# Kernel optimization log

Measured on AMD Instinct MI355X. Metric: run time of the kernel, lower is better.

## Reference

```python
import jax, jax.numpy as jnp
import numpy as np

T, B, E, H = 512, 64, 256, 256


def setup_inputs() -> dict:
    key = jax.random.key(0)
    ks = jax.random.split(key, 14)
    def p(k, shape, s=0.05):
        return jax.random.normal(k, shape, dtype=jnp.float32) * s
    return {
        "inputs": jax.random.normal(ks[0], (T, B, E), dtype=jnp.float32),
        # attention params (nn.Parameter torch.randn -> unit scale)
        "rot": jax.random.normal(ks[1], (E, E), dtype=jnp.float32),
        "ent": jax.random.normal(ks[2], (E, E), dtype=jnp.float32),
        # gate linears: stored as (in, out) so y = x @ W + b (same math as torch Linear)
        "Wf": p(ks[3], (E + H, H)), "bf": jnp.zeros((H,), jnp.float32),
        "Wi": p(ks[4], (E + H, H)), "bi": jnp.zeros((H,), jnp.float32),
        "Wu": p(ks[5], (E + H, H)), "bu": jnp.zeros((H,), jnp.float32),
        "Wo": p(ks[6], (E + H, H)), "bo": jnp.zeros((H,), jnp.float32),
        "Wc": p(ks[7], (E, H)),     "bc": jnp.zeros((H,), jnp.float32),
    }


def reference(inputs, rot, ent, Wf, bf, Wi, bi, Wu, bu, Wo, bo, Wc, bc):
    t, b, e = inputs.shape
    h = Wf.shape[1]
    # --- one-shot self-attention (ClassicalSelfAttention) ---
    inp = inputs.transpose(1, 0, 2)                       # [B,T,E]
    q = jnp.einsum('bte,ef->btf', inp, rot)
    k = jnp.einsum('bte,ef->btf', inp, ent)
    scores = jax.nn.softmax(jnp.einsum('btf,bsf->bts', q, k) / jnp.sqrt(jnp.float32(e)), axis=-1)
    context = jnp.einsum('bts,bse->bte', scores, inp).transpose(1, 0, 2)  # [T,B,E]
    # context projection is time-invariant -> precompute as one big GEMM
    ctx_proj = context @ Wc + bc                          # [T,B,H]
    # --- recurrent LSTM cell over time via scan ---
    def step(carry, xs):
        hx, cx = carry
        x, cp = xs
        combined = jnp.concatenate([x, hx + cp], axis=1)  # [B,E+H]
        f = jax.nn.sigmoid(combined @ Wf + bf)
        i = jax.nn.sigmoid(combined @ Wi + bi)
        g = jnp.tanh(combined @ Wu + bu)
        o = jax.nn.sigmoid(combined @ Wo + bo)
        cx = f * cx + i * g
        hx = o * jnp.tanh(cx)
        return (hx, cx), hx
    hx0 = jnp.zeros((b, h), inputs.dtype)
    cx0 = jnp.zeros((b, h), inputs.dtype)
    (hx, cx), outputs = jax.lax.scan(step, (hx0, cx0), (inputs, ctx_proj))
    return outputs, hx, cx
```

## Files before the change

kernel.cpp:

```cpp
#include <hip/hip_runtime.h>

#define T_ 512
#define B_ 64
#define E_ 256
#define H_ 256

typedef __attribute__((ext_vector_type(8))) short short8_t;
typedef __attribute__((ext_vector_type(4))) float floatx4;

__device__ __forceinline__ unsigned short f2bf(float f) {
  unsigned int u = __float_as_uint(f);
  u += 0x7FFFu + ((u >> 16) & 1u);
  return (unsigned short)(u >> 16);
}
__device__ __forceinline__ float bf2f(unsigned short s) {
  return __uint_as_float(((unsigned int)s) << 16);
}
__device__ __forceinline__ float fast_tanh(float x) {
  float e = __expf(-2.0f * x);
  return 2.0f / (1.0f + e) - 1.0f;
}

__global__ __launch_bounds__(256) void qk_kernel(
    const float* __restrict__ inp, const float* __restrict__ rot,
    const float* __restrict__ ent, float* __restrict__ qo, float* __restrict__ ko)
{
  __shared__ __align__(16) float As[16][136];
  __shared__ __align__(16) float B1[16][68];
  __shared__ __align__(16) float B2[16][68];
  const int tid = threadIdx.x;
  const int m0 = blockIdx.y * 128, n0 = blockIdx.x * 64;
  const int lk = tid & 15, lm = tid >> 4;
  const int ln = tid & 63, lkb = tid >> 6;
  const int tx = tid & 15, ty = tid >> 4;
  float acc1[8][4], acc2[8][4];
#pragma unroll
  for (int i = 0; i < 8; ++i)
#pragma unroll
    for (int j = 0; j < 4; ++j) { acc1[i][j] = 0.f; acc2[i][j] = 0.f; }

  for (int k0 = 0; k0 < 256; k0 += 16) {
    __syncthreads();
#pragma unroll
    for (int p = 0; p < 8; ++p) {
      int m = lm + p * 16;
      As[lk][m] = inp[(size_t)(m0 + m) * 256 + k0 + lk];
    }
#pragma unroll
    for (int p = 0; p < 4; ++p) {
      int kk = lkb + p * 4;
      B1[kk][ln] = rot[(size_t)(k0 + kk) * 256 + n0 + ln];
      B2[kk][ln] = ent[(size_t)(k0 + kk) * 256 + n0 + ln];
    }
    __syncthreads();
#pragma unroll
    for (int kk = 0; kk < 16; ++kk) {
      floatx4 a_lo = *(const floatx4*)&As[kk][ty * 8];
      floatx4 a_hi = *(const floatx4*)&As[kk][ty * 8 + 4];
      floatx4 b1v = *(const floatx4*)&B1[kk][tx * 4];
      floatx4 b2v = *(const floatx4*)&B2[kk][tx * 4];
#pragma unroll
      for (int i = 0; i < 4; ++i) {
        float alo = a_lo[i], ahi = a_hi[i];
#pragma unroll
        for (int j = 0; j < 4; ++j) {
          acc1[i][j]     += alo * b1v[j];
          acc1[i + 4][j] += ahi * b1v[j];
          acc2[i][j]     += alo * b2v[j];
          acc2[i + 4][j] += ahi * b2v[j];
        }
      }
    }
  }
#pragma unroll
  for (int i = 0; i < 8; ++i) {
    size_t row = (size_t)(m0 + ty * 8 + i);
    float4 v1 = make_float4(acc1[i][0], acc1[i][1], acc1[i][2], acc1[i][3]);
    float4 v2 = make_float4(acc2[i][0], acc2[i][1], acc2[i][2], acc2[i][3]);
    *(float4*)&qo[row * 256 + n0 + tx * 4] = v1;
    *(float4*)&ko[row * 256 + n0 + tx * 4] = v2;
  }
}

__global__ __launch_bounds__(256) void scores_kernel(
    const float* __restrict__ q, const float* __restrict__ k, float* __restrict__ S)
{
  __shared__ __align__(16) float As[16][136];
  __shared__ __align__(16) float Bs[16][68];
  const int tid = threadIdx.x;
  const int b = blockIdx.z;
  const int m0 = blockIdx.y * 128, n0 = blockIdx.x * 64;
  const int lk = tid & 15, lm = tid >> 4;
  const int tx = tid & 15, ty = tid >> 4;
  float acc[8][4];
#pragma unroll
  for (int i = 0; i < 8; ++i)
#pragma unroll
    for (int j = 0; j < 4; ++j) acc[i][j] = 0.f;

  const float* Ab = q + (size_t)b * 256;
  const float* Bb = k + (size_t)b * 256;
  for (int k0 = 0; k0 < 256; k0 += 16) {
    __syncthreads();
#pragma unroll
    for (int p = 0; p < 8; ++p) {
      int m = lm + p * 16;
      As[lk][m] = Ab[(size_t)(m0 + m) * 16384 + k0 + lk];
    }
#pragma unroll
    for (int p = 0; p < 4; ++p) {
      int n = lm + p * 16;
      Bs[lk][n] = Bb[(size_t)(n0 + n) * 16384 + k0 + lk];
    }
    __syncthreads();
#pragma unroll
    for (int kk = 0; kk < 16; ++kk) {
      floatx4 a_lo = *(const floatx4*)&As[kk][ty * 8];
      floatx4 a_hi = *(const floatx4*)&As[kk][ty * 8 + 4];
      floatx4 bv = *(const floatx4*)&Bs[kk][tx * 4];
#pragma unroll
      for (int i = 0; i < 4; ++i) {
        float alo = a_lo[i], ahi = a_hi[i];
#pragma unroll
        for (int j = 0; j < 4; ++j) {
          acc[i][j]     += alo * bv[j];
          acc[i + 4][j] += ahi * bv[j];
        }
      }
    }
  }
#pragma unroll
  for (int i = 0; i < 8; ++i) {
    size_t off = (size_t)b * 262144 + (size_t)(m0 + ty * 8 + i) * 512 + n0 + tx * 4;
    float4 v = make_float4(acc[i][0] * 0.0625f, acc[i][1] * 0.0625f,
                           acc[i][2] * 0.0625f, acc[i][3] * 0.0625f);
    *(float4*)&S[off] = v;
  }
}

__global__ __launch_bounds__(256) void softmax_kernel(float* __restrict__ S)
{
  float* p = S + (size_t)blockIdx.x * 512;
  const int tid = threadIdx.x;
  float x0 = p[tid], x1 = p[tid + 256];
  float m = fmaxf(x0, x1);
#pragma unroll
  for (int off = 32; off > 0; off >>= 1) m = fmaxf(m, __shfl_xor(m, off));
  __shared__ float red[8];
  const int wv = tid >> 6;
  if ((tid & 63) == 0) red[wv] = m;
  __syncthreads();
  m = fmaxf(fmaxf(red[0], red[1]), fmaxf(red[2], red[3]));
  float e0 = __expf(x0 - m);
  float e1 = __expf(x1 - m);
  float s = e0 + e1;
#pragma unroll
  for (int off = 32; off > 0; off >>= 1) s += __shfl_xor(s, off);
  if ((tid & 63) == 0) red[4 + wv] = s;
  __syncthreads();
  s = red[4] + red[5] + red[6] + red[7];
  float r = 1.0f / s;
  p[tid] = e0 * r;
  p[tid + 256] = e1 * r;
}

__global__ __launch_bounds__(256) void context_kernel(
    const float* __restrict__ P, const float* __restrict__ inp, float* __restrict__ ctx)
{
  __shared__ __align__(16) float As[16][136];
  __shared__ __align__(16) float Bs[16][68];
  const int tid = threadIdx.x;
  const int b = blockIdx.z;
  const int m0 = blockIdx.y * 128, e0 = blockIdx.x * 64;
  const int lk = tid & 15, lm = tid >> 4;
  const int ln = tid & 63, lkb = tid >> 6;
  const int tx = tid & 15, ty = tid >> 4;
  float acc[8][4];
#pragma unroll
  for (int i = 0; i < 8; ++i)
#pragma unroll
    for (int j = 0; j < 4; ++j) acc[i][j] = 0.f;

  const float* Ab = P + (size_t)b * 262144;
  for (int k0 = 0; k0 < 512; k0 += 16) {
    __syncthreads();
#pragma unroll
    for (int p = 0; p < 8; ++p) {
      int m = lm + p * 16;
      As[lk][m] = Ab[(size_t)(m0 + m) * 512 + k0 + lk];
    }
#pragma unroll
    for (int p = 0; p < 4; ++p) {
      int kk = lkb + p * 4;
      Bs[kk][ln] = inp[(size_t)(k0 + kk) * 16384 + b * 256 + e0 + ln];
    }
    __syncthreads();
#pragma unroll
    for (int kk = 0; kk < 16; ++kk) {
      floatx4 a_lo = *(const floatx4*)&As[kk][ty * 8];
      floatx4 a_hi = *(const floatx4*)&As[kk][ty * 8 + 4];
      floatx4 bv = *(const floatx4*)&Bs[kk][tx * 4];
#pragma unroll
      for (int i = 0; i < 4; ++i) {
        float alo = a_lo[i], ahi = a_hi[i];
#pragma unroll
        for (int j = 0; j < 4; ++j) {
          acc[i][j]     += alo * bv[j];
          acc[i + 4][j] += ahi * bv[j];
        }
      }
    }
  }
#pragma unroll
  for (int i = 0; i < 8; ++i) {
    size_t off = (size_t)(m0 + ty * 8 + i) * 16384 + (size_t)b * 256 + e0 + tx * 4;
    float4 v = make_float4(acc[i][0], acc[i][1], acc[i][2], acc[i][3]);
    *(float4*)&ctx[off] = v;
  }
}

__global__ __launch_bounds__(256) void cp_kernel(
    const float* __restrict__ ctx, const float* __restrict__ Wc,
    const float* __restrict__ bc, float* __restrict__ cp)
{
  __shared__ __align__(16) float As[16][136];
  __shared__ __align__(16) float Bs[16][68];
  const int tid = threadIdx.x;
  const int m0 = blockIdx.y * 128, n0 = blockIdx.x * 64;
  const int lk = tid & 15, lm = tid >> 4;
  const int ln = tid & 63, lkb = tid >> 6;
  const int tx = tid & 15, ty = tid >> 4;
  float acc[8][4];
#pragma unroll
  for (int i = 0; i < 8; ++i)
#pragma unroll
    for (int j = 0; j < 4; ++j) acc[i][j] = 0.f;

  for (int k0 = 0; k0 < 256; k0 += 16) {
    __syncthreads();
#pragma unroll
    for (int p = 0; p < 8; ++p) {
      int m = lm + p * 16;
      As[lk][m] = ctx[(size_t)(m0 + m) * 256 + k0 + lk];
    }
#pragma unroll
    for (int p = 0; p < 4; ++p) {
      int kk = lkb + p * 4;
      Bs[kk][ln] = Wc[(size_t)(k0 + kk) * 256 + n0 + ln];
    }
    __syncthreads();
#pragma unroll
    for (int kk = 0; kk < 16; ++kk) {
      floatx4 a_lo = *(const floatx4*)&As[kk][ty * 8];
      floatx4 a_hi = *(const floatx4*)&As[kk][ty * 8 + 4];
      floatx4 bv = *(const floatx4*)&Bs[kk][tx * 4];
#pragma unroll
      for (int i = 0; i < 4; ++i) {
        float alo = a_lo[i], ahi = a_hi[i];
#pragma unroll
        for (int j = 0; j < 4; ++j) {
          acc[i][j]     += alo * bv[j];
          acc[i + 4][j] += ahi * bv[j];
        }
      }
    }
  }
  float b0 = bc[n0 + tx * 4 + 0], b1 = bc[n0 + tx * 4 + 1];
  float b2 = bc[n0 + tx * 4 + 2], b3 = bc[n0 + tx * 4 + 3];
#pragma unroll
  for (int i = 0; i < 8; ++i) {
    size_t row = (size_t)(m0 + ty * 8 + i);
    float4 v = make_float4(acc[i][0] + b0, acc[i][1] + b1, acc[i][2] + b2, acc[i][3] + b3);
    *(float4*)&cp[row * 256 + n0 + tx * 4] = v;
  }
}

__global__ __launch_bounds__(256) void pack_w(
    const float* __restrict__ Wf, const float* __restrict__ Wi,
    const float* __restrict__ Wu, const float* __restrict__ Wo,
    const float* __restrict__ bfv, const float* __restrict__ biv,
    const float* __restrict__ buv, const float* __restrict__ bov,
    unsigned short* __restrict__ Wt, float* __restrict__ bcat)
{
  const int n = blockIdx.x;
  const int g = n >> 8, h = n & 255;
  const float* W = (g == 0) ? Wf : (g == 1) ? Wi : (g == 2) ? Wu : Wo;
  const float* bb = (g == 0) ? bfv : (g == 1) ? biv : (g == 2) ? buv : bov;
  for (int k = threadIdx.x; k < 512; k += 256)
    Wt[(size_t)n * 512 + k] = f2bf(W[(size_t)k * 256 + h]);
  if (threadIdx.x == 0) bcat[n] = bb[h];
}

__global__ __launch_bounds__(256) void gemm_pre(
    const float* __restrict__ x, const float* __restrict__ cp,
    const unsigned short* __restrict__ Wt, const float* __restrict__ bcat,
    unsigned short* __restrict__ pre)
{
  __shared__ __align__(16) unsigned short As[64 * 40];
  __shared__ __align__(16) unsigned short Bs[64 * 40];
  const int tid = threadIdx.x;
  const int n0 = blockIdx.x * 64, m0 = blockIdx.y * 64;
  const int lane = tid & 63, wv = tid >> 6;
  const int lm = lane & 15, qd = lane >> 4;
  const int sr = tid >> 2, sk = (tid & 3) * 8;
  floatx4 acc[4] = {{0.f,0.f,0.f,0.f},{0.f,0.f,0.f,0.f},
                    {0.f,0.f,0.f,0.f},{0.f,0.f,0.f,0.f}};
  for (int k0 = 0; k0 < 512; k0 += 32) {
    const float* Asrc = (k0 < 256)
        ? (x  + (size_t)(m0 + sr) * 256 + k0 + sk)
        : (cp + (size_t)(m0 + sr) * 256 + (k0 - 256) + sk);
    float4 a0 = *(const float4*)Asrc;
    float4 a1 = *(const float4*)(Asrc + 4);
    short8_t av;
    av[0] = (short)f2bf(a0.x); av[1] = (short)f2bf(a0.y);
    av[2] = (short)f2bf(a0.z); av[3] = (short)f2bf(a0.w);
    av[4] = (short)f2bf(a1.x); av[5] = (short)f2bf(a1.y);
    av[6] = (short)f2bf(a1.z); av[7] = (short)f2bf(a1.w);
    short8_t bv = *(const short8_t*)&Wt[(size_t)(n0 + sr) * 512 + k0 + sk];
    *(short8_t*)&As[sr * 40 + sk] = av;
    *(short8_t*)&Bs[sr * 40 + sk] = bv;
    __syncthreads();
    short8_t af = *(const short8_t*)&As[(wv * 16 + lm) * 40 + qd * 8];
#pragma unroll
    for (int nt = 0; nt < 4; ++nt) {
      short8_t bf = *(const short8_t*)&Bs[(nt * 16 + lm) * 40 + qd * 8];
      acc[nt] = __builtin_amdgcn_mfma_f32_16x16x32_bf16(af, bf, acc[nt], 0, 0, 0);
    }
    __syncthreads();
  }
#pragma unroll
  for (int nt = 0; nt < 4; ++nt) {
    int col = n0 + nt * 16 + lm;
    float bb = bcat[col];
    int col2 = ((col & 255) << 2) | (col >> 8);
#pragma unroll
    for (int r = 0; r < 4; ++r) {
      int row = m0 + wv * 16 + qd * 4 + r;
      pre[(size_t)row * 1024 + col2] = f2bf(acc[nt][r] + bb);
    }
  }
}

__global__ __launch_bounds__(512, 2) void scan_kernel(
    const unsigned short* __restrict__ pre,
    const unsigned short* __restrict__ Wt,
    float* __restrict__ out)
{
  __shared__ __align__(16) unsigned short ldsB[8 * 18 * 512];
  __shared__ __align__(16) unsigned short hl[2][9 * 264];
  const int tid = threadIdx.x;
  const int bg = blockIdx.x;
  const int lane = tid & 63;
  const int w = tid >> 6;
  const int qd = lane >> 4;
  const int lm = lane & 15;

  {
    unsigned long long* z = (unsigned long long*)hl;
    for (int i = tid; i < 1188; i += 512) z[i] = 0ull;
  }

  short8_t wreg[46];
#pragma unroll
  for (int nt = 0; nt < 8; ++nt) {
#pragma unroll
    for (int kc = 0; kc < 8; ++kc) {
      const int idx = nt * 8 + kc;
      const int g = nt >> 1, cg2 = nt & 1;
      short8_t v = *(const short8_t*)&Wt[
          (size_t)(g * 256 + w * 32 + cg2 * 16 + lm) * 512 + 256 + kc * 32 + qd * 8];
      if (idx < 46) wreg[idx] = v;
      else *(short8_t*)&ldsB[(w * 18 + (idx - 46)) * 512 + lane * 8] = v;
    }
  }

  const int rh = lane >> 5;
  const int cg2d = (lane >> 4) & 1;
  const int c15 = lane & 15;
  const int hc = w * 32 + cg2d * 16 + c15;
  const int srcl = rh * 16 + c15;
  const int arow = (lm < 8) ? lm : 8;
  const int aoff = arow * 264 + qd * 8;

  const unsigned long long* pq = (const unsigned long long*)pre;
  float cst[4] = {0.f, 0.f, 0.f, 0.f};

  __syncthreads();

#pragma unroll 1
  for (int t = 0; t < 512; ++t) {
    const unsigned short* hbR = hl[t & 1];

    unsigned long long pcur[4];
    {
      size_t base = (size_t)(t * 64 + bg * 8 + rh * 4) * 256 + hc;
#pragma unroll
      for (int r = 0; r < 4; ++r)
        pcur[r] = pq[base + (size_t)r * 256];
    }

    floatx4 acc[8];
#pragma unroll
    for (int nt = 0; nt < 8; ++nt) acc[nt] = {0.f, 0.f, 0.f, 0.f};
#pragma unroll
    for (int kc = 0; kc < 8; ++kc) {
      short8_t av = *(const short8_t*)&hbR[aoff + kc * 32];
#pragma unroll
      for (int nt = 0; nt < 8; ++nt) {
        const int idx = nt * 8 + kc;
        short8_t bf;
        if (idx < 46) bf = wreg[idx];
        else bf = *(const short8_t*)&ldsB[(w * 18 + (idx - 46)) * 512 + lane * 8];
        acc[nt] = __builtin_amdgcn_mfma_f32_16x16x32_bf16(av, bf, acc[nt], 0, 0, 0);
      }
    }

    unsigned short* hbW = hl[(t + 1) & 1];
#pragma unroll
    for (int r = 0; r < 4; ++r) {
      float vg[4];
#pragma unroll
      for (int g = 0; g < 4; ++g) {
        float v0 = __shfl(acc[g * 2 + 0][r], srcl);
        float v1 = __shfl(acc[g * 2 + 1][r], srcl);
        vg[g] = cg2d ? v1 : v0;
      }
      unsigned long long pv = pcur[r];
      float xf = vg[0] + bf2f((unsigned short)pv);
      float xi = vg[1] + bf2f((unsigned short)(pv >> 16));
      float xu = vg[2] + bf2f((unsigned short)(pv >> 32));
      float xo = vg[3] + bf2f((unsigned short)(pv >> 48));
      float fg = 1.0f / (1.0f + __expf(-xf));
      float ig = 1.0f / (1.0f + __expf(-xi));
      float gg = fast_tanh(xu);
      float og = 1.0f / (1.0f + __expf(-xo));
      float cc = fg * cst[r] + ig * gg;
      cst[r] = cc;
      float hh = og * fast_tanh(cc);
      const int lr = rh * 4 + r;
      hbW[lr * 264 + hc] = f2bf(hh);
      out[(size_t)t * 16384 + (size_t)(bg * 8 + lr) * 256 + hc] = hh;
      if (t == 511) {
        const size_t hoff = (size_t)512 * 16384 + (size_t)(bg * 8 + lr) * 256 + hc;
        out[hoff] = hh;
        out[hoff + 16384] = cc;
      }
    }
    __syncthreads();
  }
}

extern "C" void kernel_launch(void* const* d_in, const int* in_sizes, int n_in,
                              void* d_out, int out_size, void* d_ws, size_t ws_size,
                              hipStream_t stream)
{
  const float* inputs = (const float*)d_in[0];
  const float* rot = (const float*)d_in[1];
  const float* ent = (const float*)d_in[2];
  const float* Wf = (const float*)d_in[3];
  const float* bf_ = (const float*)d_in[4];
  const float* Wi = (const float*)d_in[5];
  const float* bi_ = (const float*)d_in[6];
  const float* Wu = (const float*)d_in[7];
  const float* bu_ = (const float*)d_in[8];
  const float* Wo = (const float*)d_in[9];
  const float* bo_ = (const float*)d_in[10];
  const float* Wc = (const float*)d_in[11];
  const float* bc_ = (const float*)d_in[12];
  float* out = (float*)d_out;

  char* ws = (char*)d_ws;
  float* q  = (float*)(ws);
  float* kb = (float*)(ws + (size_t)32 * 1024 * 1024);
  float* S  = (float*)(ws + (size_t)64 * 1024 * 1024);
  unsigned short* pre = (unsigned short*)S;
  float* ctx = q;
  float* cp  = kb;
  unsigned short* Wcat = (unsigned short*)ws;
  float* bcat = (float*)(ws + (size_t)1048576);

  qk_kernel<<<dim3(4, 256), 256, 0, stream>>>(inputs, rot, ent, q, kb);
  scores_kernel<<<dim3(8, 4, 64), 256, 0, stream>>>(q, kb, S);
  softmax_kernel<<<dim3(32768), 256, 0, stream>>>(S);
  context_kernel<<<dim3(4, 4, 64), 256, 0, stream>>>(S, inputs, ctx);
  cp_kernel<<<dim3(4, 256), 256, 0, stream>>>(ctx, Wc, bc_, cp);
  pack_w<<<dim3(1024), 256, 0, stream>>>(Wf, Wi, Wu, Wo, bf_, bi_, bu_, bo_,
                                         Wcat, bcat);
  gemm_pre<<<dim3(16, 512), 256, 0, stream>>>(inputs, cp, Wcat, bcat, pre);
  scan_kernel<<<dim3(8), 512, 0, stream>>>(pre, Wcat, out);
}
```

Measured before the change: 2.064 ms.

## Restructure LSTM scan to 4 blocks of 16 waves streaming weights from global

The recurrent scan now runs 4 blocks of 1024 threads, each handling 16 batch rows with 16 waves, and each wave computes all four gates for 16 hidden columns. The gate values therefore land in the same lane and the cross-lane shuffles go away. Weights are no longer kept in registers and LDS. Instead they are reloaded from global/L2 every timestep, double-buffered one k-chunk ahead. This removes the shuffle and gate-assembly overhead and the LDS weight staging, at the cost of repeated weight loads from cache on the serial critical path and fewer parallel blocks.

```diff
diff --git a/kernel.cpp b/kernel.cpp
--- a/kernel.cpp
+++ b/kernel.cpp
@@ -341,13 +341,12 @@
   }
 }
 
-__global__ __launch_bounds__(512, 2) void scan_kernel(
+__global__ __launch_bounds__(1024, 4) void scan_kernel(
     const unsigned short* __restrict__ pre,
     const unsigned short* __restrict__ Wt,
     float* __restrict__ out)
 {
-  __shared__ __align__(16) unsigned short ldsB[8 * 18 * 512];
-  __shared__ __align__(16) unsigned short hl[2][9 * 264];
+  __shared__ __align__(16) unsigned short hl[2][16 * 264];
   const int tid = threadIdx.x;
   const int bg = blockIdx.x;
   const int lane = tid & 63;
@@ -357,79 +356,75 @@
 
   {
     unsigned long long* z = (unsigned long long*)hl;
-    for (int i = tid; i < 1188; i += 512) z[i] = 0ull;
-  }
-
-  short8_t wreg[46];
-#pragma unroll
-  for (int nt = 0; nt < 8; ++nt) {
-#pragma unroll
-    for (int kc = 0; kc < 8; ++kc) {
-      const int idx = nt * 8 + kc;
-      const int g = nt >> 1, cg2 = nt & 1;
-      short8_t v = *(const short8_t*)&Wt[
-          (size_t)(g * 256 + w * 32 + cg2 * 16 + lm) * 512 + 256 + kc * 32 + qd * 8];
-      if (idx < 46) wreg[idx] = v;
-      else *(short8_t*)&ldsB[(w * 18 + (idx - 46)) * 512 + lane * 8] = v;
-    }
-  }
-
-  const int rh = lane >> 5;
-  const int cg2d = (lane >> 4) & 1;
-  const int c15 = lane & 15;
-  const int hc = w * 32 + cg2d * 16 + c15;
-  const int srcl = rh * 16 + c15;
-  const int arow = (lm < 8) ? lm : 8;
-  const int aoff = arow * 264 + qd * 8;
+    for (int i = tid; i < 2112; i += 1024) z[i] = 0ull;
+  }
+
+  const unsigned short* wb[4];
+#pragma unroll
+  for (int g = 0; g < 4; ++g)
+    wb[g] = Wt + (size_t)(g * 256 + w * 16 + lm) * 512 + 256 + qd * 8;
 
   const unsigned long long* pq = (const unsigned long long*)pre;
+  const int orow0 = bg * 16 + qd * 4;
+  const int hcol = w * 16 + lm;
   float cst[4] = {0.f, 0.f, 0.f, 0.f};
+
+  short8_t Ba[4], Bb[4];
+#pragma unroll
+  for (int g = 0; g < 4; ++g) Ba[g] = *(const short8_t*)(wb[g]);
 
   __syncthreads();
 
 #pragma unroll 1
   for (int t = 0; t < 512; ++t) {
     const unsigned short* hbR = hl[t & 1];
+    unsigned short* hbW = hl[(t + 1) & 1];
 
     unsigned long long pcur[4];
     {
-      size_t base = (size_t)(t * 64 + bg * 8 + rh * 4) * 256 + hc;
+      size_t base = (size_t)(t * 64 + orow0) * 256 + hcol;
 #pragma unroll
       for (int r = 0; r < 4; ++r)
         pcur[r] = pq[base + (size_t)r * 256];
     }
 
-    floatx4 acc[8];
-#pragma unroll
-    for (int nt = 0; nt < 8; ++nt) acc[nt] = {0.f, 0.f, 0.f, 0.f};
+    floatx4 acc[4] = {{0.f,0.f,0.f,0.f},{0.f,0.f,0.f,0.f},
+                      {0.f,0.f,0.f,0.f},{0.f,0.f,0.f,0.f}};
 #pragma unroll
     for (int kc = 0; kc < 8; ++kc) {
-      short8_t av = *(const short8_t*)&hbR[aoff + kc * 32];
-#pragma unroll
-      for (int nt = 0; nt < 8; ++nt) {
-        const int idx = nt * 8 + kc;
-        short8_t bf;
-        if (idx < 46) bf = wreg[idx];
-        else bf = *(const short8_t*)&ldsB[(w * 18 + (idx - 46)) * 512 + lane * 8];
-        acc[nt] = __builtin_amdgcn_mfma_f32_16x16x32_bf16(av, bf, acc[nt], 0, 0, 0);
-      }
-    }
-
-    unsigned short* hbW = hl[(t + 1) & 1];
+      if (kc < 7) {
+        if ((kc & 1) == 0) {
+#pragma unroll
+          for (int g = 0; g < 4; ++g)
+            Bb[g] = *(const short8_t*)(wb[g] + (kc + 1) * 32);
+        } else {
+#pragma unroll
+          for (int g = 0; g < 4; ++g)
+            Ba[g] = *(const short8_t*)(wb[g] + (kc + 1) * 32);
+        }
+      }
+      short8_t av = *(const short8_t*)&hbR[lm * 264 + kc * 32 + qd * 8];
+      if ((kc & 1) == 0) {
+#pragma unroll
+        for (int g = 0; g < 4; ++g)
+          acc[g] = __builtin_amdgcn_mfma_f32_16x16x32_bf16(av, Ba[g], acc[g], 0, 0, 0);
+      } else {
+#pragma unroll
+        for (int g = 0; g < 4; ++g)
+          acc[g] = __builtin_amdgcn_mfma_f32_16x16x32_bf16(av, Bb[g], acc[g], 0, 0, 0);
+      }
+    }
+
+#pragma unroll
+    for (int g = 0; g < 4; ++g) Ba[g] = *(const short8_t*)(wb[g]);
+
 #pragma unroll
     for (int r = 0; r < 4; ++r) {
-      float vg[4];
-#pragma unroll
-      for (int g = 0; g < 4; ++g) {
-        float v0 = __shfl(acc[g * 2 + 0][r], srcl);
-        float v1 = __shfl(acc[g * 2 + 1][r], srcl);
-        vg[g] = cg2d ? v1 : v0;
-      }
       unsigned long long pv = pcur[r];
-      float xf = vg[0] + bf2f((unsigned short)pv);
-      float xi = vg[1] + bf2f((unsigned short)(pv >> 16));
-      float xu = vg[2] + bf2f((unsigned short)(pv >> 32));
-      float xo = vg[3] + bf2f((unsigned short)(pv >> 48));
+      float xf = acc[0][r] + bf2f((unsigned short)pv);
+      float xi = acc[1][r] + bf2f((unsigned short)(pv >> 16));
+      float xu = acc[2][r] + bf2f((unsigned short)(pv >> 32));
+      float xo = acc[3][r] + bf2f((unsigned short)(pv >> 48));
       float fg = 1.0f / (1.0f + __expf(-xf));
       float ig = 1.0f / (1.0f + __expf(-xi));
       float gg = fast_tanh(xu);
@@ -437,11 +432,10 @@
       float cc = fg * cst[r] + ig * gg;
       cst[r] = cc;
       float hh = og * fast_tanh(cc);
-      const int lr = rh * 4 + r;
-      hbW[lr * 264 + hc] = f2bf(hh);
-      out[(size_t)t * 16384 + (size_t)(bg * 8 + lr) * 256 + hc] = hh;
+      hbW[(qd * 4 + r) * 264 + hcol] = f2bf(hh);
+      out[(size_t)t * 16384 + (size_t)(orow0 + r) * 256 + hcol] = hh;
       if (t == 511) {
-        const size_t hoff = (size_t)512 * 16384 + (size_t)(bg * 8 + lr) * 256 + hc;
+        const size_t hoff = (size_t)512 * 16384 + (size_t)(orow0 + r) * 256 + hcol;
         out[hoff] = hh;
         out[hoff + 16384] = cc;
       }
@@ -487,5 +481,5 @@
   pack_w<<<dim3(1024), 256, 0, stream>>>(Wf, Wi, Wu, Wo, bf_, bi_, bu_, bo_,
                                          Wcat, bcat);
   gemm_pre<<<dim3(16, 512), 256, 0, stream>>>(inputs, cp, Wcat, bcat, pre);
-  scan_kernel<<<dim3(8), 512, 0, stream>>>(pre, Wcat, out);
-}
+  scan_kernel<<<dim3(4), 1024, 0, stream>>>(pre, Wcat, out);
+}
```

Measured after the change: 4.737 ms. 2.3x slower.
